# Kernel optimization log

Hardware: AMD Instinct MI355X
Metric: run time of the kernel (lower is better)

## Reference

```python
import jax, jax.numpy as jnp
import numpy as np

RATIO = 0.12
# Per output channel (after shuffle [4,5,6,7,0,1,2,3] applied to the first entry of each
# selectable_directions group): (pos_x, pos_y, neg_x, neg_y) offsets into the 3x3 stencil.
# conv2d with a +1/-1 sparse kernel == padded[pos] - padded[neg] neighbor difference.
OFFSETS = [
    (1, 0, 2, 2),  # old filter 4: dirs [9,4]
    (0, 2, 1, 0),  # old filter 5: dirs [4,3]
    (2, 1, 0, 2),  # old filter 6: dirs [3,8]
    (0, 0, 2, 1),  # old filter 7: dirs [8,1]
    (1, 2, 1, 1),  # old filter 0: dirs [5,6]
    (0, 1, 1, 1),  # old filter 1: dirs [5,2]
    (0, 2, 1, 1),  # old filter 2: dirs [5,3]
    (0, 0, 1, 1),  # old filter 3: dirs [5,1]
]


def setup_inputs() -> dict:
    key = jax.random.key(0)
    img = jax.random.uniform(key, (16, 3, 512, 512), dtype=jnp.float32)
    return {"img": img}


def reference(img):
    B, C, H, W = img.shape
    # channel max -> [B,1,H,W]
    img_v = jnp.max(img, axis=1, keepdims=True)
    # replicate pad by 1 on each spatial side -> [B,1,H+2,W+2]
    padded = jnp.pad(img_v, ((0, 0), (0, 0), (1, 1), (1, 1)), mode='edge')
    # per-image dynamic range -> [1,B,1,1,1] (matches unsqueeze(0) in torch code)
    rng = (jnp.max(img_v, axis=(2, 3), keepdims=True)
           - jnp.min(img_v, axis=(2, 3), keepdims=True))[None]
    # sparse +1/-1 3x3 conv as 8 neighbor differences -> [8,B,H,W]
    diffs = jnp.stack(
        [padded[:, 0, px:px + H, py:py + W] - padded[:, 0, nx:nx + H, ny:ny + W]
         for (px, py, nx, ny) in OFFSETS],
        axis=0,
    )
    pos = jnp.maximum(diffs, 0.0)   # all_img_v * (all_img_v >= 0)
    neg = jnp.maximum(-diffs, 0.0)  # -all_img_v * (all_img_v < 0)
    out = jnp.stack([pos, neg], axis=2)  # [8,B,2,H,W]
    return (out >= rng * RATIO).astype(jnp.float32)
```

## Files before the change

### kernel.cpp

```cpp
#include <hip/hip_runtime.h>
#include <cstdint>
#include <cstddef>

typedef float f32x4 __attribute__((ext_vector_type(4)));

constexpr int BB = 16, CC = 3, HH = 512, WW = 512;
constexpr int HW = HH * WW;
constexpr float RATIO = 0.12f;
constexpr int TR = 16;
constexpr int TILES = HH / TR;


__global__ __launch_bounds__(256) void k1_minmax(
        const float* __restrict__ img, float* __restrict__ pmin,
        float* __restrict__ pmax) {
    int t    = blockIdx.x * 256 + threadIdx.x;
    int off4 = t << 2;
    int b    = off4 / HW;
    int off  = off4 - b * HW;
    const float* base = img + (size_t)b * CC * HW + off;
    f32x4 c0 = *(const f32x4*)(base);
    f32x4 c1 = *(const f32x4*)(base + HW);
    f32x4 c2 = *(const f32x4*)(base + 2 * HW);
    f32x4 v;
    v.x = fmaxf(fmaxf(c0.x, c1.x), c2.x);
    v.y = fmaxf(fmaxf(c0.y, c1.y), c2.y);
    v.z = fmaxf(fmaxf(c0.z, c1.z), c2.z);
    v.w = fmaxf(fmaxf(c0.w, c1.w), c2.w);

    float mn = fminf(fminf(v.x, v.y), fminf(v.z, v.w));
    float mx = fmaxf(fmaxf(v.x, v.y), fmaxf(v.z, v.w));
    #pragma unroll
    for (int s = 32; s > 0; s >>= 1) {
        mn = fminf(mn, __shfl_xor(mn, s, 64));
        mx = fmaxf(mx, __shfl_xor(mx, s, 64));
    }
    __shared__ float smn[4], smx[4];
    int wave = threadIdx.x >> 6;
    if ((threadIdx.x & 63) == 0) { smn[wave] = mn; smx[wave] = mx; }
    __syncthreads();
    if (threadIdx.x == 0) {
        pmin[blockIdx.x] = fminf(fminf(smn[0], smn[1]), fminf(smn[2], smn[3]));
        pmax[blockIdx.x] = fmaxf(fmaxf(smx[0], smx[1]), fmaxf(smx[2], smx[3]));
    }
}

__global__ __launch_bounds__(256, 4) void k2_edges(
        const float* __restrict__ img, const float* __restrict__ pmin,
        const float* __restrict__ pmax, float* __restrict__ out) {
    int bid = blockIdx.x;
    int x   = bid & 7;
    int m   = bid >> 3;
    int f   = m & 7;
    int g   = ((m >> 3) << 3) + x;
    int b    = g >> 5;
    int tile = g & 31;
    int t    = threadIdx.x;

    __shared__ float sred[8];
    {
        float mlo = pmin[(b << 8) + t];
        float mhi = pmax[(b << 8) + t];
        #pragma unroll
        for (int s = 32; s > 0; s >>= 1) {
            mlo = fminf(mlo, __shfl_xor(mlo, s, 64));
            mhi = fmaxf(mhi, __shfl_xor(mhi, s, 64));
        }
        if ((t & 63) == 0) { sred[t >> 6] = mlo; sred[4 + (t >> 6)] = mhi; }
    }

    __shared__ float ld[18 * WW];
    int tile0 = tile * TR;
    const float* ib = img + (size_t)b * CC * HW;
    #pragma unroll
    for (int s = 0; s < 9; ++s) {
        int v  = t + (s << 8);
        int vr = v >> 7;
        int vc = (v & 127) << 2;
        int g2 = min(max(tile0 - 1 + vr, 0), HH - 1);
        const float* rb = ib + (size_t)g2 * WW + vc;
        f32x4 a0 = *(const f32x4*)(rb);
        f32x4 a1 = *(const f32x4*)(rb + HW);
        f32x4 a2 = *(const f32x4*)(rb + 2 * HW);
        f32x4 q;
        q.x = fmaxf(fmaxf(a0.x, a1.x), a2.x);
        q.y = fmaxf(fmaxf(a0.y, a1.y), a2.y);
        q.z = fmaxf(fmaxf(a0.z, a1.z), a2.z);
        q.w = fmaxf(fmaxf(a0.w, a1.w), a2.w);
        *(f32x4*)&ld[vr * WW + vc] = q;
    }
    __syncthreads();
    float thr = (fmaxf(fmaxf(sred[4], sred[5]), fmaxf(sred[6], sred[7]))
               - fminf(fminf(sred[0], sred[1]), fminf(sred[2], sred[3]))) * RATIO;

    int c  = (t & 127) << 2;
    int cl = max(c - 1, 0), cr = min(c + 4, WW - 1);
    int rb2 = t >> 7;
    size_t planep = (size_t)((f * BB + b) * 2) * HW;
    float* outp = out + planep;
    float* outn = out + planep + HW;

    #pragma unroll
    for (int j = 0; j < 8; ++j) {
        int orow = (j << 1) + rb2;
        const float* T = &ld[orow * WW];
        const float* M = &ld[(orow + 1) * WW];
        const float* P = &ld[(orow + 2) * WW];
        float vt[6], vm[6], vp[6];
        { f32x4 q = *(const f32x4*)(T + c);
          vt[0] = T[cl]; vt[1] = q.x; vt[2] = q.y; vt[3] = q.z; vt[4] = q.w; vt[5] = T[cr]; }
        { f32x4 q = *(const f32x4*)(M + c);
          vm[0] = M[cl]; vm[1] = q.x; vm[2] = q.y; vm[3] = q.z; vm[4] = q.w; vm[5] = M[cr]; }
        { f32x4 q = *(const f32x4*)(P + c);
          vp[0] = P[cl]; vp[1] = q.x; vp[2] = q.y; vp[3] = q.z; vp[4] = q.w; vp[5] = P[cr]; }

        float d0, d1, d2, d3;
        switch (f) {
            case 0: d0 = vm[0]-vp[2]; d1 = vm[1]-vp[3]; d2 = vm[2]-vp[4]; d3 = vm[3]-vp[5]; break;
            case 1: d0 = vt[2]-vm[0]; d1 = vt[3]-vm[1]; d2 = vt[4]-vm[2]; d3 = vt[5]-vm[3]; break;
            case 2: d0 = vp[1]-vt[2]; d1 = vp[2]-vt[3]; d2 = vp[3]-vt[4]; d3 = vp[4]-vt[5]; break;
            case 3: d0 = vt[0]-vp[1]; d1 = vt[1]-vp[2]; d2 = vt[2]-vp[3]; d3 = vt[3]-vp[4]; break;
            case 4: d0 = vm[2]-vm[1]; d1 = vm[3]-vm[2]; d2 = vm[4]-vm[3]; d3 = vm[5]-vm[4]; break;
            case 5: d0 = vt[1]-vm[1]; d1 = vt[2]-vm[2]; d2 = vt[3]-vm[3]; d3 = vt[4]-vm[4]; break;
            case 6: d0 = vt[2]-vm[1]; d1 = vt[3]-vm[2]; d2 = vt[4]-vm[3]; d3 = vt[5]-vm[4]; break;
            default:d0 = vt[0]-vm[1]; d1 = vt[1]-vm[2]; d2 = vt[2]-vm[3]; d3 = vt[3]-vm[4]; break;
        }
        f32x4 qp, qn;
        qp.x = (fmaxf(d0, 0.f) >= thr) ? 1.f : 0.f;
        qp.y = (fmaxf(d1, 0.f) >= thr) ? 1.f : 0.f;
        qp.z = (fmaxf(d2, 0.f) >= thr) ? 1.f : 0.f;
        qp.w = (fmaxf(d3, 0.f) >= thr) ? 1.f : 0.f;
        qn.x = (fmaxf(-d0, 0.f) >= thr) ? 1.f : 0.f;
        qn.y = (fmaxf(-d1, 0.f) >= thr) ? 1.f : 0.f;
        qn.z = (fmaxf(-d2, 0.f) >= thr) ? 1.f : 0.f;
        qn.w = (fmaxf(-d3, 0.f) >= thr) ? 1.f : 0.f;

        size_t po = (size_t)(tile0 + orow) * WW + c;
        *(f32x4*)(outp + po) = qp;
        *(f32x4*)(outn + po) = qn;
    }
}

extern "C" void kernel_launch(void* const* d_in, const int* in_sizes, int n_in,
                              void* d_out, int out_size, void* d_ws, size_t ws_size,
                              hipStream_t stream) {
    const float* img = (const float*)d_in[0];
    float* out  = (float*)d_out;
    float* pmin = (float*)d_ws;
    float* pmax = (float*)((char*)d_ws + 16384);

    k1_minmax<<<4096, 256, 0, stream>>>(img, pmin, pmax);
    k2_edges<<<8 * BB * TILES, 256, 0, stream>>>(img, pmin, pmax, out);
}
```

Before: 65.58 us.

## Fuse min/max reduction into edge kernel with atomic per-image grid barrier

Drops the separate min/max pass. Each block now computes the channel-max tile, contributes its min/max through atomics, and spins until all 64 blocks of its image have arrived before computing the threshold. Each block now emits 4 filters instead of 1, so every input tile is loaded twice rather than eight times, and the full-image read of the first kernel disappears. The cost is a spin barrier that depends on all 1024 blocks being co-resident (256 CUs times 4 blocks per CU), which risks deadlock if occupancy is lower. A tiny init kernel launch is also added.

```diff
diff --git a/kernel.cpp b/kernel.cpp
--- a/kernel.cpp
+++ b/kernel.cpp
@@ -8,70 +8,32 @@
 constexpr int HW = HH * WW;
 constexpr float RATIO = 0.12f;
 constexpr int TR = 16;
-constexpr int TILES = HH / TR;
+constexpr int NBLK = 1024;
 
 
-__global__ __launch_bounds__(256) void k1_minmax(
-        const float* __restrict__ img, float* __restrict__ pmin,
-        float* __restrict__ pmax) {
-    int t    = blockIdx.x * 256 + threadIdx.x;
-    int off4 = t << 2;
-    int b    = off4 / HW;
-    int off  = off4 - b * HW;
-    const float* base = img + (size_t)b * CC * HW + off;
-    f32x4 c0 = *(const f32x4*)(base);
-    f32x4 c1 = *(const f32x4*)(base + HW);
-    f32x4 c2 = *(const f32x4*)(base + 2 * HW);
-    f32x4 v;
-    v.x = fmaxf(fmaxf(c0.x, c1.x), c2.x);
-    v.y = fmaxf(fmaxf(c0.y, c1.y), c2.y);
-    v.z = fmaxf(fmaxf(c0.z, c1.z), c2.z);
-    v.w = fmaxf(fmaxf(c0.w, c1.w), c2.w);
-
-    float mn = fminf(fminf(v.x, v.y), fminf(v.z, v.w));
-    float mx = fmaxf(fmaxf(v.x, v.y), fmaxf(v.z, v.w));
-    #pragma unroll
-    for (int s = 32; s > 0; s >>= 1) {
-        mn = fminf(mn, __shfl_xor(mn, s, 64));
-        mx = fmaxf(mx, __shfl_xor(mx, s, 64));
-    }
-    __shared__ float smn[4], smx[4];
-    int wave = threadIdx.x >> 6;
-    if ((threadIdx.x & 63) == 0) { smn[wave] = mn; smx[wave] = mx; }
-    __syncthreads();
-    if (threadIdx.x == 0) {
-        pmin[blockIdx.x] = fminf(fminf(smn[0], smn[1]), fminf(smn[2], smn[3]));
-        pmax[blockIdx.x] = fmaxf(fmaxf(smx[0], smx[1]), fmaxf(smx[2], smx[3]));
-    }
+__global__ void initc(unsigned int* mmc) {
+    int i = threadIdx.x;
+    if (i < 16)      mmc[i] = 0x7F800000u;
+    else if (i < 48) mmc[i] = 0u;
 }
 
-__global__ __launch_bounds__(256, 4) void k2_edges(
-        const float* __restrict__ img, const float* __restrict__ pmin,
-        const float* __restrict__ pmax, float* __restrict__ out) {
-    int bid = blockIdx.x;
-    int x   = bid & 7;
-    int m   = bid >> 3;
-    int f   = m & 7;
-    int g   = ((m >> 3) << 3) + x;
+__global__ __launch_bounds__(256, 4) void fused(
+        const float* __restrict__ img, float* __restrict__ out,
+        unsigned int* __restrict__ mmc) {
+    int bid  = blockIdx.x;
+    int h    = bid & 1;
+    int g    = bid >> 1;
     int b    = g >> 5;
     int tile = g & 31;
     int t    = threadIdx.x;
+    int tile0 = tile * TR;
 
+    __shared__ float ld[(TR + 2) * WW];
     __shared__ float sred[8];
-    {
-        float mlo = pmin[(b << 8) + t];
-        float mhi = pmax[(b << 8) + t];
-        #pragma unroll
-        for (int s = 32; s > 0; s >>= 1) {
-            mlo = fminf(mlo, __shfl_xor(mlo, s, 64));
-            mhi = fmaxf(mhi, __shfl_xor(mhi, s, 64));
-        }
-        if ((t & 63) == 0) { sred[t >> 6] = mlo; sred[4 + (t >> 6)] = mhi; }
-    }
+    __shared__ float sthr;
 
-    __shared__ float ld[18 * WW];
-    int tile0 = tile * TR;
     const float* ib = img + (size_t)b * CC * HW;
+    float mn = 3.4e38f, mx = 0.0f;
     #pragma unroll
     for (int s = 0; s < 9; ++s) {
         int v  = t + (s << 8);
@@ -88,56 +50,86 @@
         q.z = fmaxf(fmaxf(a0.z, a1.z), a2.z);
         q.w = fmaxf(fmaxf(a0.w, a1.w), a2.w);
         *(f32x4*)&ld[vr * WW + vc] = q;
+        mn = fminf(mn, fminf(fminf(q.x, q.y), fminf(q.z, q.w)));
+        mx = fmaxf(mx, fmaxf(fmaxf(q.x, q.y), fmaxf(q.z, q.w)));
+    }
+    #pragma unroll
+    for (int s = 32; s > 0; s >>= 1) {
+        mn = fminf(mn, __shfl_xor(mn, s, 64));
+        mx = fmaxf(mx, __shfl_xor(mx, s, 64));
+    }
+    int wave = t >> 6;
+    if ((t & 63) == 0) { sred[wave] = mn; sred[4 + wave] = mx; }
+    __syncthreads();
+
+    if (t == 0) {
+        float m0 = fminf(fminf(sred[0], sred[1]), fminf(sred[2], sred[3]));
+        float m1 = fmaxf(fmaxf(sred[4], sred[5]), fmaxf(sred[6], sred[7]));
+        atomicMin(&mmc[b],      __float_as_uint(m0));
+        atomicMax(&mmc[16 + b], __float_as_uint(m1));
+        __hip_atomic_fetch_add(&mmc[32 + b], 1u, __ATOMIC_ACQ_REL,
+                               __HIP_MEMORY_SCOPE_AGENT);
+        while (__hip_atomic_load(&mmc[32 + b], __ATOMIC_ACQUIRE,
+                                 __HIP_MEMORY_SCOPE_AGENT) < 64u)
+            __builtin_amdgcn_s_sleep(2);
+        unsigned lo = __hip_atomic_load(&mmc[b], __ATOMIC_ACQUIRE,
+                                        __HIP_MEMORY_SCOPE_AGENT);
+        unsigned hi = __hip_atomic_load(&mmc[16 + b], __ATOMIC_ACQUIRE,
+                                        __HIP_MEMORY_SCOPE_AGENT);
+        sthr = (__uint_as_float(hi) - __uint_as_float(lo)) * RATIO;
     }
     __syncthreads();
-    float thr = (fmaxf(fmaxf(sred[4], sred[5]), fmaxf(sred[6], sred[7]))
-               - fminf(fminf(sred[0], sred[1]), fminf(sred[2], sred[3]))) * RATIO;
+    float thr = sthr;
 
     int c  = (t & 127) << 2;
     int cl = max(c - 1, 0), cr = min(c + 4, WW - 1);
     int rb2 = t >> 7;
-    size_t planep = (size_t)((f * BB + b) * 2) * HW;
-    float* outp = out + planep;
-    float* outn = out + planep + HW;
 
     #pragma unroll
-    for (int j = 0; j < 8; ++j) {
-        int orow = (j << 1) + rb2;
-        const float* T = &ld[orow * WW];
-        const float* M = &ld[(orow + 1) * WW];
-        const float* P = &ld[(orow + 2) * WW];
-        float vt[6], vm[6], vp[6];
-        { f32x4 q = *(const f32x4*)(T + c);
-          vt[0] = T[cl]; vt[1] = q.x; vt[2] = q.y; vt[3] = q.z; vt[4] = q.w; vt[5] = T[cr]; }
-        { f32x4 q = *(const f32x4*)(M + c);
-          vm[0] = M[cl]; vm[1] = q.x; vm[2] = q.y; vm[3] = q.z; vm[4] = q.w; vm[5] = M[cr]; }
-        { f32x4 q = *(const f32x4*)(P + c);
-          vp[0] = P[cl]; vp[1] = q.x; vp[2] = q.y; vp[3] = q.z; vp[4] = q.w; vp[5] = P[cr]; }
+    for (int fi = 0; fi < 4; ++fi) {
+        int f = (h << 2) + fi;
+        size_t planep = (size_t)((f * BB + b) * 2) * HW;
+        float* outp = out + planep;
+        float* outn = outp + HW;
+        #pragma unroll
+        for (int j = 0; j < 8; ++j) {
+            int orow = (j << 1) + rb2;
+            const float* T = &ld[orow * WW];
+            const float* M = &ld[(orow + 1) * WW];
+            const float* P = &ld[(orow + 2) * WW];
+            float vt[6], vm[6], vp[6];
+            { f32x4 q = *(const f32x4*)(T + c);
+              vt[0] = T[cl]; vt[1] = q.x; vt[2] = q.y; vt[3] = q.z; vt[4] = q.w; vt[5] = T[cr]; }
+            { f32x4 q = *(const f32x4*)(M + c);
+              vm[0] = M[cl]; vm[1] = q.x; vm[2] = q.y; vm[3] = q.z; vm[4] = q.w; vm[5] = M[cr]; }
+            { f32x4 q = *(const f32x4*)(P + c);
+              vp[0] = P[cl]; vp[1] = q.x; vp[2] = q.y; vp[3] = q.z; vp[4] = q.w; vp[5] = P[cr]; }
 
-        float d0, d1, d2, d3;
-        switch (f) {
-            case 0: d0 = vm[0]-vp[2]; d1 = vm[1]-vp[3]; d2 = vm[2]-vp[4]; d3 = vm[3]-vp[5]; break;
-            case 1: d0 = vt[2]-vm[0]; d1 = vt[3]-vm[1]; d2 = vt[4]-vm[2]; d3 = vt[5]-vm[3]; break;
-            case 2: d0 = vp[1]-vt[2]; d1 = vp[2]-vt[3]; d2 = vp[3]-vt[4]; d3 = vp[4]-vt[5]; break;
-            case 3: d0 = vt[0]-vp[1]; d1 = vt[1]-vp[2]; d2 = vt[2]-vp[3]; d3 = vt[3]-vp[4]; break;
-            case 4: d0 = vm[2]-vm[1]; d1 = vm[3]-vm[2]; d2 = vm[4]-vm[3]; d3 = vm[5]-vm[4]; break;
-            case 5: d0 = vt[1]-vm[1]; d1 = vt[2]-vm[2]; d2 = vt[3]-vm[3]; d3 = vt[4]-vm[4]; break;
-            case 6: d0 = vt[2]-vm[1]; d1 = vt[3]-vm[2]; d2 = vt[4]-vm[3]; d3 = vt[5]-vm[4]; break;
-            default:d0 = vt[0]-vm[1]; d1 = vt[1]-vm[2]; d2 = vt[2]-vm[3]; d3 = vt[3]-vm[4]; break;
+            float d0, d1, d2, d3;
+            switch (f) {
+                case 0: d0 = vm[0]-vp[2]; d1 = vm[1]-vp[3]; d2 = vm[2]-vp[4]; d3 = vm[3]-vp[5]; break;
+                case 1: d0 = vt[2]-vm[0]; d1 = vt[3]-vm[1]; d2 = vt[4]-vm[2]; d3 = vt[5]-vm[3]; break;
+                case 2: d0 = vp[1]-vt[2]; d1 = vp[2]-vt[3]; d2 = vp[3]-vt[4]; d3 = vp[4]-vt[5]; break;
+                case 3: d0 = vt[0]-vp[1]; d1 = vt[1]-vp[2]; d2 = vt[2]-vp[3]; d3 = vt[3]-vp[4]; break;
+                case 4: d0 = vm[2]-vm[1]; d1 = vm[3]-vm[2]; d2 = vm[4]-vm[3]; d3 = vm[5]-vm[4]; break;
+                case 5: d0 = vt[1]-vm[1]; d1 = vt[2]-vm[2]; d2 = vt[3]-vm[3]; d3 = vt[4]-vm[4]; break;
+                case 6: d0 = vt[2]-vm[1]; d1 = vt[3]-vm[2]; d2 = vt[4]-vm[3]; d3 = vt[5]-vm[4]; break;
+                default:d0 = vt[0]-vm[1]; d1 = vt[1]-vm[2]; d2 = vt[2]-vm[3]; d3 = vt[3]-vm[4]; break;
+            }
+            f32x4 qp, qn;
+            qp.x = (fmaxf(d0, 0.f) >= thr) ? 1.f : 0.f;
+            qp.y = (fmaxf(d1, 0.f) >= thr) ? 1.f : 0.f;
+            qp.z = (fmaxf(d2, 0.f) >= thr) ? 1.f : 0.f;
+            qp.w = (fmaxf(d3, 0.f) >= thr) ? 1.f : 0.f;
+            qn.x = (fmaxf(-d0, 0.f) >= thr) ? 1.f : 0.f;
+            qn.y = (fmaxf(-d1, 0.f) >= thr) ? 1.f : 0.f;
+            qn.z = (fmaxf(-d2, 0.f) >= thr) ? 1.f : 0.f;
+            qn.w = (fmaxf(-d3, 0.f) >= thr) ? 1.f : 0.f;
+
+            size_t po = (size_t)(tile0 + orow) * WW + c;
+            *(f32x4*)(outp + po) = qp;
+            *(f32x4*)(outn + po) = qn;
         }
-        f32x4 qp, qn;
-        qp.x = (fmaxf(d0, 0.f) >= thr) ? 1.f : 0.f;
-        qp.y = (fmaxf(d1, 0.f) >= thr) ? 1.f : 0.f;
-        qp.z = (fmaxf(d2, 0.f) >= thr) ? 1.f : 0.f;
-        qp.w = (fmaxf(d3, 0.f) >= thr) ? 1.f : 0.f;
-        qn.x = (fmaxf(-d0, 0.f) >= thr) ? 1.f : 0.f;
-        qn.y = (fmaxf(-d1, 0.f) >= thr) ? 1.f : 0.f;
-        qn.z = (fmaxf(-d2, 0.f) >= thr) ? 1.f : 0.f;
-        qn.w = (fmaxf(-d3, 0.f) >= thr) ? 1.f : 0.f;
-
-        size_t po = (size_t)(tile0 + orow) * WW + c;
-        *(f32x4*)(outp + po) = qp;
-        *(f32x4*)(outn + po) = qn;
     }
 }
 
@@ -145,10 +137,9 @@
                               void* d_out, int out_size, void* d_ws, size_t ws_size,
                               hipStream_t stream) {
     const float* img = (const float*)d_in[0];
-    float* out  = (float*)d_out;
-    float* pmin = (float*)d_ws;
-    float* pmax = (float*)((char*)d_ws + 16384);
+    float* out = (float*)d_out;
+    unsigned int* mmc = (unsigned int*)d_ws;
 
-    k1_minmax<<<4096, 256, 0, stream>>>(img, pmin, pmax);
-    k2_edges<<<8 * BB * TILES, 256, 0, stream>>>(img, pmin, pmax, out);
+    initc<<<1, 64, 0, stream>>>(mmc);
+    fused<<<NBLK, 256, 0, stream>>>(img, out, mmc);
 }
```

New measurement: 175.3 us. 167% more time.
